# Kernel tuning notes

Hardware: AMD Instinct MI355X
Metric: run time of the kernel (lower is better)

The kernel has to match this reference:

```python
import jax, jax.numpy as jnp
import numpy as np

# Module constants (hardcoded in the torch source)
N = 4            # _NUM_QUBITS
D = 1            # _QAOA_DEPTH
H = 6            # number of Hamiltonian terms (free dim, chosen = C(4,2))
S = 2 * D * (H + 1)  # num_states in _qaoa_matrix

I2   = jnp.eye(2, dtype=jnp.complex64)
PX   = jnp.array([[0, 1], [1, 0]], dtype=jnp.complex64)
PZ   = jnp.array([[1, 0], [0, -1]], dtype=jnp.complex64)
UNIF = 0.5 * jnp.ones((2, 2), dtype=jnp.complex64)
ONES = jnp.ones((2, 2), dtype=jnp.complex64)

def _gray_states():
    # Replicates the ret-flip loop in _qaoa_matrix: at step i flip bit log2(i & ~(i-1)).
    ret = np.zeros(S, dtype=bool)
    out = []
    for i in range(S):
        if i:
            ind = (i & -i).bit_length() - 1
            ret[ind] = not ret[ind]
        out.append(ret.copy())
    return np.stack(out)  # [S, S] static bool

GRAY = _gray_states()

def _half_factor(offset, beta0, gamma0, weights, flags):
    # Elementwise 2x2 factor applied to every ring matrix by _apply_qaoa_matrix
    # for one half (generator starting at `offset`). All multiplies in the
    # original are ELEMENTWISE (torch `*`), hence commutative -> one fused factor.
    xflag = jnp.asarray(GRAY[:, offset])                    # [S] beta/PauliX kron flag
    hfl   = jnp.asarray(GRAY[:, offset + 1: offset + 1 + H])  # [S, H] hamiltonian kron flags
    theta = gamma0 * weights                                # [H]
    c = jnp.where(hfl, -1j * jnp.sin(theta), jnp.cos(theta).astype(jnp.complex64))  # [S,H]
    s_h = jnp.prod(c, axis=1)                               # [S] scalar applied to each ring
    Fb = jnp.where(xflag[:, None, None],
                   (-1j * jnp.sin(beta0)) * PX,
                   jnp.cos(beta0) * ONES)                    # [S,2,2]
    eff = hfl[:, :, None] & flags[None, :, :]               # [S,H,N]: apply PauliZ on qubit n for term j
    Zf = jnp.where(eff[..., None, None], PZ, ONES)          # [S,H,N,2,2]
    Zp = jnp.prod(Zf, axis=1)                               # [S,N,2,2]
    return s_h[:, None, None, None] * Fb[:, None] * Zp      # [S,N,2,2]


def setup_inputs() -> dict:
    key = jax.random.key(0)
    k1, k2, k3, k4 = jax.random.split(key, 4)
    weights = jax.random.normal(k1, (H,), dtype=jnp.float32)
    flags = jax.random.randint(k2, (H, N), 0, 2).astype(bool)
    beta = jax.random.normal(k3, (D,), dtype=jnp.float32)
    gamma = jax.random.normal(k4, (D,), dtype=jnp.float32)
    return {"weights": weights, "flags": flags, "beta": beta, "gamma": gamma}


def reference(weights, flags, beta, gamma):
    b0, g0 = beta[0], gamma[0]
    # D=1, so params[-1] == params[0]: both halves use the same (beta, gamma).
    F1 = _half_factor(0, b0, g0, weights, flags)             # first half (offset 0)
    F2 = _half_factor(D * (H + 1), b0, g0, weights, flags)   # second half
    base = jnp.where(flags[:, :, None, None], PZ, I2)        # [H,N,2,2] initial ring per term
    # ring[t,s,n] = base * F1 * UNIFORM * F2 (all elementwise 2x2)
    ring = base[:, None] * F1[None] * UNIF * F2[None]        # [H,S,N,2,2]
    tr = ring[..., 0, 0] + ring[..., 1, 1]                   # trace of each 2x2 -> [H,S,N]
    temp = jnp.prod(tr, axis=-1)                             # [H,S]
    return jnp.sum(weights.astype(jnp.complex64)[:, None] * temp)  # complex scalar
```

## Files before the change

### kernel.cpp

```cpp
#include <hip/hip_runtime.h>
#include <math.h>


#define NQ 4
#define NH 6
#define NS 14

struct cplx { double re, im; };
__device__ __forceinline__ cplx cmul(cplx a, cplx b) {
    return { a.re * b.re - a.im * b.im, a.re * b.im + a.im * b.re };
}
__device__ __forceinline__ cplx cscale(cplx a, double s) {
    return { a.re * s, a.im * s };
}

__global__ void qaoa_kernel(const float* __restrict__ w,
                            const int*   __restrict__ flags,
                            const float* __restrict__ beta,
                            const float* __restrict__ gamma,
                            float* __restrict__ out, int out_size)
{
    __shared__ double s_re[128];
    __shared__ double s_im[128];
    const int tid = threadIdx.x;

    const double cb = cos((double)beta[0]);
    const double g0 = (double)gamma[0];
    double cth[NH], sth[NH];
#pragma unroll
    for (int j = 0; j < NH; ++j) {
        double th = g0 * (double)w[j];
        cth[j] = cos(th);
        sth[j] = sin(th);
    }

    double re = 0.0, im = 0.0;
    if (tid < NH * NS) {
        const int h = tid / NS;
        const int s = tid % NS;
        const unsigned g = (unsigned)s ^ ((unsigned)s >> 1);

        const unsigned x1   = g & 1u;
        const unsigned hfl1 = (g >> 1) & 0x3Fu;
        const unsigned x2   = (g >> 7) & 1u;
        const unsigned hfl2 = (g >> 8) & 0x3Fu;

        cplx sh1 = {1.0, 0.0}, sh2 = {1.0, 0.0};
#pragma unroll
        for (int j = 0; j < NH; ++j) {
            cplx c1 = ((hfl1 >> j) & 1u) ? cplx{0.0, -sth[j]} : cplx{cth[j], 0.0};
            cplx c2 = ((hfl2 >> j) & 1u) ? cplx{0.0, -sth[j]} : cplx{cth[j], 0.0};
            sh1 = cmul(sh1, c1);
            sh2 = cmul(sh2, c2);
        }

        const double fb1 = x1 ? 0.0 : cb;
        const double fb2 = x2 ? 0.0 : cb;
        const cplx  s12  = cmul(sh1, sh2);
        const double fbb = 0.5 * fb1 * fb2;

        cplx temp = {1.0, 0.0};
#pragma unroll
        for (int n = 0; n < NQ; ++n) {
            int cnt1 = 0, cnt2 = 0;
#pragma unroll
            for (int j = 0; j < NH; ++j) {
                const int f = (flags[j * NQ + n] != 0) ? 1 : 0;
                cnt1 += (int)((hfl1 >> j) & 1u) & f;
                cnt2 += (int)((hfl2 >> j) & 1u) & f;
            }
            const double z1  = (cnt1 & 1) ? -1.0 : 1.0;
            const double z2  = (cnt2 & 1) ? -1.0 : 1.0;
            const double b11 = (flags[h * NQ + n] != 0) ? -1.0 : 1.0;
            const double scal = fbb * (1.0 + b11 * z1 * z2);
            const cplx tr = cscale(s12, scal);
            temp = cmul(temp, tr);
        }
        const double wh = (double)w[h];
        re = wh * temp.re;
        im = wh * temp.im;
    }

    s_re[tid] = re;
    s_im[tid] = im;
    __syncthreads();
#pragma unroll
    for (int off = 64; off > 0; off >>= 1) {
        if (tid < off) {
            s_re[tid] += s_re[tid + off];
            s_im[tid] += s_im[tid + off];
        }
        __syncthreads();
    }
    if (tid == 0) {
        if (out_size > 0) out[0] = (float)s_re[0];
        if (out_size > 1) out[1] = (float)s_im[0];
    }
}

extern "C" void kernel_launch(void* const* d_in, const int* in_sizes, int n_in,
                              void* d_out, int out_size, void* d_ws, size_t ws_size,
                              hipStream_t stream) {
    const float* w     = (const float*)d_in[0];
    const int*   flags = (const int*)d_in[1];
    const float* beta  = (const float*)d_in[2];
    const float* gamma = (const float*)d_in[3];
    float* out = (float*)d_out;
    (void)in_sizes; (void)n_in; (void)d_ws; (void)ws_size;
    qaoa_kernel<<<1, 128, 0, stream>>>(w, flags, beta, gamma, out, out_size);
}
```

Baseline: 9.639 us.

## Switch to fp32 math and single-wavefront shuffle reduction

Replaces double-precision arithmetic with float, cutting the slow fp64 transcendentals and multiplies. Uses one 64-lane wavefront that handles up to two items per lane, with a shuffle reduction in place of the shared-memory tree reduction and its barriers. Flags are preloaded into registers. A redundant __sincosf call is left in, overwritten by sinf/cosf. Float precision may slightly change numerical accuracy of the complex sum.

Measured after the change: 9.571 us. About the same (-0.7%).

```diff
diff --git a/kernel.cpp b/kernel.cpp
--- a/kernel.cpp
+++ b/kernel.cpp
@@ -5,13 +5,58 @@
 #define NQ 4
 #define NH 6
 #define NS 14
+#define NITEMS (NH * NS)
 
-struct cplx { double re, im; };
-__device__ __forceinline__ cplx cmul(cplx a, cplx b) {
+struct cplxf { float re, im; };
+__device__ __forceinline__ cplxf cmulf(cplxf a, cplxf b) {
     return { a.re * b.re - a.im * b.im, a.re * b.im + a.im * b.re };
 }
-__device__ __forceinline__ cplx cscale(cplx a, double s) {
-    return { a.re * s, a.im * s };
+
+__device__ __forceinline__ void accum_item(int item,
+                                           const float* cth, const float* sth,
+                                           float cb, const int* fl, const float* wl,
+                                           float& re, float& im)
+{
+    const int h = item / NS;
+    const int s = item % NS;
+    const unsigned g = (unsigned)s ^ ((unsigned)s >> 1);
+
+    const unsigned x1   = g & 1u;
+    const unsigned hfl1 = (g >> 1) & 0x3Fu;
+    const unsigned x2   = (g >> 7) & 1u;
+    const unsigned hfl2 = (g >> 8) & 0x3Fu;
+
+    cplxf sh1 = {1.f, 0.f}, sh2 = {1.f, 0.f};
+#pragma unroll
+    for (int j = 0; j < NH; ++j) {
+        cplxf c1 = ((hfl1 >> j) & 1u) ? cplxf{0.f, -sth[j]} : cplxf{cth[j], 0.f};
+        cplxf c2 = ((hfl2 >> j) & 1u) ? cplxf{0.f, -sth[j]} : cplxf{cth[j], 0.f};
+        sh1 = cmulf(sh1, c1);
+        sh2 = cmulf(sh2, c2);
+    }
+
+    const float fb1 = x1 ? 0.f : cb;
+    const float fb2 = x2 ? 0.f : cb;
+    const cplxf s12 = cmulf(sh1, sh2);
+    const float fbb = 0.5f * fb1 * fb2;
+
+    cplxf temp = {1.f, 0.f};
+#pragma unroll
+    for (int n = 0; n < NQ; ++n) {
+        int cnt1 = 0, cnt2 = 0;
+#pragma unroll
+        for (int j = 0; j < NH; ++j) {
+            const int f = fl[j * NQ + n];
+            cnt1 += (int)((hfl1 >> j) & 1u) & f;
+            cnt2 += (int)((hfl2 >> j) & 1u) & f;
+        }
+        const float z12 = ((cnt1 ^ cnt2) & 1) ? -1.f : 1.f;
+        const float b11 = fl[h * NQ + n] ? -1.f : 1.f;
+        const float scal = fbb * (1.f + b11 * z12);
+        temp = cmulf(temp, cplxf{s12.re * scal, s12.im * scal});
+    }
+    re += wl[h] * temp.re;
+    im += wl[h] * temp.im;
 }
 
 __global__ void qaoa_kernel(const float* __restrict__ w,
@@ -20,81 +65,35 @@
                             const float* __restrict__ gamma,
                             float* __restrict__ out, int out_size)
 {
-    __shared__ double s_re[128];
-    __shared__ double s_im[128];
-    const int tid = threadIdx.x;
+    const int lane = threadIdx.x;
 
-    const double cb = cos((double)beta[0]);
-    const double g0 = (double)gamma[0];
-    double cth[NH], sth[NH];
+    const float cb = cosf(beta[0]);
+    const float g0 = gamma[0];
+    float cth[NH], sth[NH], wl[NH];
+    int fl[NH * NQ];
 #pragma unroll
     for (int j = 0; j < NH; ++j) {
-        double th = g0 * (double)w[j];
-        cth[j] = cos(th);
-        sth[j] = sin(th);
+        wl[j] = w[j];
+        __sincosf(g0 * wl[j], &sth[j], &cth[j]);
+        sth[j] = sinf(g0 * wl[j]);
+        cth[j] = cosf(g0 * wl[j]);
     }
+#pragma unroll
+    for (int k = 0; k < NH * NQ; ++k) fl[k] = (flags[k] != 0) ? 1 : 0;
 
-    double re = 0.0, im = 0.0;
-    if (tid < NH * NS) {
-        const int h = tid / NS;
-        const int s = tid % NS;
-        const unsigned g = (unsigned)s ^ ((unsigned)s >> 1);
+    float re = 0.f, im = 0.f;
+    accum_item(lane, cth, sth, cb, fl, wl, re, im);
+    if (lane < NITEMS - 64)
+        accum_item(lane + 64, cth, sth, cb, fl, wl, re, im);
 
-        const unsigned x1   = g & 1u;
-        const unsigned hfl1 = (g >> 1) & 0x3Fu;
-        const unsigned x2   = (g >> 7) & 1u;
-        const unsigned hfl2 = (g >> 8) & 0x3Fu;
-
-        cplx sh1 = {1.0, 0.0}, sh2 = {1.0, 0.0};
 #pragma unroll
-        for (int j = 0; j < NH; ++j) {
-            cplx c1 = ((hfl1 >> j) & 1u) ? cplx{0.0, -sth[j]} : cplx{cth[j], 0.0};
-            cplx c2 = ((hfl2 >> j) & 1u) ? cplx{0.0, -sth[j]} : cplx{cth[j], 0.0};
-            sh1 = cmul(sh1, c1);
-            sh2 = cmul(sh2, c2);
-        }
-
-        const double fb1 = x1 ? 0.0 : cb;
-        const double fb2 = x2 ? 0.0 : cb;
-        const cplx  s12  = cmul(sh1, sh2);
-        const double fbb = 0.5 * fb1 * fb2;
-
-        cplx temp = {1.0, 0.0};
-#pragma unroll
-        for (int n = 0; n < NQ; ++n) {
-            int cnt1 = 0, cnt2 = 0;
-#pragma unroll
-            for (int j = 0; j < NH; ++j) {
-                const int f = (flags[j * NQ + n] != 0) ? 1 : 0;
-                cnt1 += (int)((hfl1 >> j) & 1u) & f;
-                cnt2 += (int)((hfl2 >> j) & 1u) & f;
-            }
-            const double z1  = (cnt1 & 1) ? -1.0 : 1.0;
-            const double z2  = (cnt2 & 1) ? -1.0 : 1.0;
-            const double b11 = (flags[h * NQ + n] != 0) ? -1.0 : 1.0;
-            const double scal = fbb * (1.0 + b11 * z1 * z2);
-            const cplx tr = cscale(s12, scal);
-            temp = cmul(temp, tr);
-        }
-        const double wh = (double)w[h];
-        re = wh * temp.re;
-        im = wh * temp.im;
+    for (int off = 32; off > 0; off >>= 1) {
+        re += __shfl_down(re, off, 64);
+        im += __shfl_down(im, off, 64);
     }
-
-    s_re[tid] = re;
-    s_im[tid] = im;
-    __syncthreads();
-#pragma unroll
-    for (int off = 64; off > 0; off >>= 1) {
-        if (tid < off) {
-            s_re[tid] += s_re[tid + off];
-            s_im[tid] += s_im[tid + off];
-        }
-        __syncthreads();
-    }
-    if (tid == 0) {
-        if (out_size > 0) out[0] = (float)s_re[0];
-        if (out_size > 1) out[1] = (float)s_im[0];
+    if (lane == 0) {
+        if (out_size > 0) out[0] = re;
+        if (out_size > 1) out[1] = im;
     }
 }
 
@@ -107,5 +106,5 @@
     const float* gamma = (const float*)d_in[3];
     float* out = (float*)d_out;
     (void)in_sizes; (void)n_in; (void)d_ws; (void)ws_size;
-    qaoa_kernel<<<1, 128, 0, stream>>>(w, flags, beta, gamma, out, out_size);
+    qaoa_kernel<<<1, 64, 0, stream>>>(w, flags, beta, gamma, out, out_size);
 }
```
